# Performance work log

Measured on AMD Instinct MI355X. Metric: run time of the kernel, lower is better.

Reference implementation:

```python
import jax, jax.numpy as jnp
import numpy as np

N = 40000
E = 640000
IN = 128
H = 8
F = 16  # out_features per head; H*F == IN for the residual
NEG_SLOPE = 0.2
BN_EPS = 1e-5
SOFTMAX_EPS = 1e-16


def setup_inputs() -> dict:
    key = jax.random.key(0)
    ks = jax.random.split(key, 7)
    x = jax.random.normal(ks[0], (N, IN), dtype=jnp.float32)
    edge_index = jax.random.randint(ks[1], (2, E), 0, N, dtype=jnp.int32)
    # GATConv parameters (glorot-ish scale)
    W = jax.random.normal(ks[2], (IN, H * F), dtype=jnp.float32) * (1.0 / np.sqrt(IN))
    att_src = jax.random.normal(ks[3], (H, F), dtype=jnp.float32) * (1.0 / np.sqrt(F))
    att_dst = jax.random.normal(ks[4], (H, F), dtype=jnp.float32) * (1.0 / np.sqrt(F))
    bias = jnp.zeros((H * F,), dtype=jnp.float32)
    bn_gamma = jnp.ones((H * F,), dtype=jnp.float32)
    bn_beta = jnp.zeros((H * F,), dtype=jnp.float32)
    return {"x": x, "edge_index": edge_index, "W": W, "att_src": att_src,
            "att_dst": att_dst, "bias": bias, "bn_gamma": bn_gamma, "bn_beta": bn_beta}


def _gat_layer(x, src, dst, W, att_src, att_dst, bias, bn_gamma, bn_beta):
    n = x.shape[0]
    xp = (x @ W).reshape(n, H, F)                      # [N,H,F] transformed features
    a_s = jnp.einsum('nhf,hf->nh', xp, att_src)        # [N,H]
    a_d = jnp.einsum('nhf,hf->nh', xp, att_dst)
    e = jax.nn.leaky_relu(a_s[src] + a_d[dst], NEG_SLOPE)   # [E,H] per-edge logits
    # segment softmax over edges sharing the same destination node
    m = jax.ops.segment_max(e, dst, num_segments=n)    # [N,H]
    m = jnp.where(jnp.isfinite(m), m, 0.0)             # guard isolated nodes
    p = jnp.exp(e - m[dst])
    s = jax.ops.segment_sum(p, dst, num_segments=n)    # [N,H]
    alpha = p / (s[dst] + SOFTMAX_EPS)                 # [E,H]
    # scatter-aggregate messages
    msg = alpha[:, :, None] * xp[src]                  # [E,H,F]
    out = jax.ops.segment_sum(msg, dst, num_segments=n)  # [N,H,F]
    h = out.reshape(n, H * F) + bias
    # BatchNorm1d (training-mode batch statistics, biased variance)
    mean = h.mean(axis=0)
    var = h.var(axis=0)
    h = (h - mean) * jax.lax.rsqrt(var + BN_EPS) * bn_gamma + bn_beta
    h = jax.nn.relu(h)
    return h + x                                        # residual (dropout p=0 -> identity)


def reference(x, edge_index, W, att_src, att_dst, bias, bn_gamma, bn_beta):
    n = x.shape[0]
    loops = jnp.arange(n, dtype=edge_index.dtype)
    src = jnp.concatenate([edge_index[0], loops])       # add self-loops (GATConv default)
    dst = jnp.concatenate([edge_index[1], loops])
    return _gat_layer(x, src, dst, W, att_src, att_dst, bias, bn_gamma, bn_beta)
```

## Files before the change

kernel.cpp:

```cpp
#include <hip/hip_runtime.h>
#include <math.h>


constexpr float NEG_SLOPE = 0.2f;
constexpr float BN_EPS = 1e-5f;
constexpr float SM_EPS = 1e-16f;
constexpr int SLOTS = 96;

typedef __attribute__((ext_vector_type(8))) short short8;
typedef __attribute__((ext_vector_type(4))) float f32x4;

__device__ inline unsigned bf16rne(float f) {
    unsigned b = __float_as_uint(f);
    return (b + 0x7fffu + ((b >> 16) & 1u)) >> 16;
}

__global__ __launch_bounds__(256) void k_init(
    const float* __restrict__ W, const float* __restrict__ att_src,
    const float* __restrict__ att_dst, unsigned short* __restrict__ Wtg,
    int* __restrict__ zbase, int zcount)
{
    int b = blockIdx.x;
    if (b < 64) {
        int idx = b * 256 + threadIdx.x;
        int k = idx >> 7, nc = idx & 127;
        Wtg[nc * 128 + k] = (unsigned short)bf16rne(W[idx]);
    } else if (b < 72) {
        int c = (b - 64) * 16 + (threadIdx.x >> 4);
        int j = threadIdx.x & 15;
        int h = j & 7;
        const float* att = (j < 8) ? att_src : att_dst;
        float v = 0.f;
#pragma unroll
        for (int f = 0; f < 16; ++f)
            v += W[c * 128 + h * 16 + f] * att[h * 16 + f];
        Wtg[(128 + j) * 128 + c] = (unsigned short)bf16rne(v);
    } else {
        int idx = (b - 72) * 256 + threadIdx.x;
        if (idx < zcount) zbase[idx] = 0;
    }
}

__global__ __launch_bounds__(256) void k_gemm(
    const float* __restrict__ x, const unsigned short* __restrict__ Wtg,
    const int* __restrict__ ei, int E,
    unsigned* __restrict__ xpb, float* __restrict__ a_s, float* __restrict__ a_d,
    int* __restrict__ deg, unsigned short* __restrict__ csr_src, int n,
    int ntiles)
{
    if ((int)blockIdx.x >= ntiles) {
        const int t = (blockIdx.x - ntiles) * 256 + threadIdx.x;
        if (t < E) {
            int dst = ei[E + t];
            int src = ei[t];
            int slot = atomicAdd(&deg[dst], 1);
            csr_src[(size_t)dst * SLOTS + slot] = (unsigned short)src;
        } else if (t - E < n) {
            int node = t - E;
            int slot = atomicAdd(&deg[node], 1);
            csr_src[(size_t)node * SLOTS + slot] = (unsigned short)node;
        }
        return;
    }

    const int tid = threadIdx.x;
    const int lane = tid & 63;
    const int wid = tid >> 6;
    const int quad = lane >> 4;
    const int l16 = lane & 15;
    const int row = blockIdx.x * 64 + wid * 16 + l16;

    const float4* x4 = (const float4*)x;
    short8 afrag[4];
#pragma unroll
    for (int kt = 0; kt < 4; ++kt) {
        float4 f0 = make_float4(0.f, 0.f, 0.f, 0.f), f1 = f0;
        if (row < n) {
            f0 = x4[(size_t)row * 32 + kt * 8 + quad * 2];
            f1 = x4[(size_t)row * 32 + kt * 8 + quad * 2 + 1];
        }
        short8 a;
        a[0] = (short)bf16rne(f0.x); a[1] = (short)bf16rne(f0.y);
        a[2] = (short)bf16rne(f0.z); a[3] = (short)bf16rne(f0.w);
        a[4] = (short)bf16rne(f1.x); a[5] = (short)bf16rne(f1.y);
        a[6] = (short)bf16rne(f1.z); a[7] = (short)bf16rne(f1.w);
        afrag[kt] = a;
    }

    f32x4 acc[9];
#pragma unroll
    for (int ct = 0; ct < 9; ++ct) acc[ct] = (f32x4){0.f, 0.f, 0.f, 0.f};

#pragma unroll
    for (int ct = 0; ct < 9; ++ct) {
#pragma unroll
        for (int kt = 0; kt < 4; ++kt) {
            short8 b = *(const short8*)&Wtg[(size_t)(ct * 16 + l16) * 128 + kt * 32 + quad * 8];
            acc[ct] = __builtin_amdgcn_mfma_f32_16x16x32_bf16(afrag[kt], b, acc[ct], 0, 0, 0);
        }
    }

    const int rowbase = blockIdx.x * 64 + wid * 16 + quad * 4;
#pragma unroll
    for (int ct = 0; ct < 8; ++ct) {
#pragma unroll
        for (int r = 0; r < 4; ++r) {
            float val = acc[ct][r];
            float other = __shfl_xor(val, 1);
            int orow = rowbase + r;
            if (!(lane & 1) && orow < n) {
                unsigned u = bf16rne(val) | (bf16rne(other) << 16);
                xpb[(size_t)orow * 64 + ct * 8 + (l16 >> 1)] = u;
            }
        }
    }
#pragma unroll
    for (int r = 0; r < 4; ++r) {
        int orow = rowbase + r;
        if (orow < n) {
            float val = acc[8][r];
            if (l16 < 8) a_s[(size_t)orow * 8 + l16] = val;
            else         a_d[(size_t)orow * 8 + (l16 - 8)] = val;
        }
    }
}

__global__ __launch_bounds__(256) void k_gather(
    const int* __restrict__ deg, const unsigned short* __restrict__ csr_src,
    const float* __restrict__ a_s, const float* __restrict__ a_d,
    const unsigned* __restrict__ xpb, unsigned* __restrict__ aggb, int n)
{
    int node = blockIdx.x * 4 + (threadIdx.x >> 6);
    if (node >= n) return;
    int lane = threadIdx.x & 63;
    int h = lane >> 3;
    float ad = a_d[(size_t)node * 8 + h];
    const unsigned short* rowp = csr_src + (size_t)node * SLOTS;
    int cnt = deg[node];
    float acc0 = 0.f, acc1 = 0.f, s = 0.f;

    for (int slot = 0; slot < cnt; slot += 8) {
        int sx[8]; float w[8]; unsigned u[8];
#pragma unroll
        for (int j = 0; j < 8; ++j) {
            int sj = slot + j;
            sx[j] = rowp[sj < cnt ? sj : cnt - 1];
        }
#pragma unroll
        for (int j = 0; j < 8; ++j) w[j] = a_s[(size_t)sx[j] * 8 + h];
#pragma unroll
        for (int j = 0; j < 8; ++j) u[j] = xpb[(size_t)sx[j] * 64 + lane];
#pragma unroll
        for (int j = 0; j < 8; ++j) {
            float v = w[j] + ad;
            v = v > 0.f ? v : NEG_SLOPE * v;
            float p = __expf(v);
            p = (slot + j < cnt) ? p : 0.f;
            s += p;
            acc0 = fmaf(p, __uint_as_float(u[j] << 16), acc0);
            acc1 = fmaf(p, __uint_as_float(u[j] & 0xffff0000u), acc1);
        }
    }
    float inv = 1.0f / (s + SM_EPS);
    aggb[(size_t)node * 64 + lane] = bf16rne(acc0 * inv) | (bf16rne(acc1 * inv) << 16);
}

__global__ __launch_bounds__(256) void k_bnstats(
    const unsigned* __restrict__ aggb, int n, float* __restrict__ stats)
{
    __shared__ float red[4][256];
    const int cp = threadIdx.x & 63;
    const int rg = threadIdx.x >> 6;
    float s0 = 0.f, s1 = 0.f, q0 = 0.f, q1 = 0.f;
    for (int r = blockIdx.x * 4 + rg; r < n; r += gridDim.x * 4) {
        unsigned u = aggb[(size_t)r * 64 + cp];
        float v0 = __uint_as_float(u << 16);
        float v1 = __uint_as_float(u & 0xffff0000u);
        s0 += v0; q0 += v0 * v0;
        s1 += v1; q1 += v1 * v1;
    }
    red[rg][cp * 2] = s0;       red[rg][cp * 2 + 1] = s1;
    red[rg][128 + cp * 2] = q0; red[rg][128 + cp * 2 + 1] = q1;
    __syncthreads();
    int idx = threadIdx.x;
    float v = red[0][idx] + red[1][idx] + red[2][idx] + red[3][idx];
    if (idx < 128) atomicAdd(&stats[idx], v);
    else           atomicAdd(&stats[128 + (idx - 128)], v);
}

__global__ __launch_bounds__(256) void k_final(
    const unsigned* __restrict__ aggb, const float* __restrict__ gamma,
    const float* __restrict__ beta, const float* __restrict__ stats,
    const float* __restrict__ x, float* __restrict__ out, int n)
{
    int i4 = blockIdx.x * 256 + threadIdx.x;
    int total4 = n * 32;
    if (i4 >= total4) return;
    int c4 = (i4 & 31) * 4;
    float invn = 1.0f / (float)n;
    uint2 au = ((const uint2*)aggb)[i4];
    float av[4] = { __uint_as_float(au.x << 16), __uint_as_float(au.x & 0xffff0000u),
                    __uint_as_float(au.y << 16), __uint_as_float(au.y & 0xffff0000u) };
    float4 xv = ((const float4*)x)[i4];
    float4 o;
#pragma unroll
    for (int j = 0; j < 4; ++j) {
        int c = c4 + j;
        float mean = stats[c] * invn;
        float var = stats[128 + c] * invn - mean * mean;
        float v = (av[j] - mean) * rsqrtf(var + BN_EPS) * gamma[c] + beta[c];
        v = fmaxf(v, 0.f);
        (&o.x)[j] = v + (&xv.x)[j];
    }
    ((float4*)out)[i4] = o;
}

extern "C" void kernel_launch(void* const* d_in, const int* in_sizes, int n_in,
                              void* d_out, int out_size, void* d_ws, size_t ws_size,
                              hipStream_t stream)
{
    const float* x        = (const float*)d_in[0];
    const int*   ei       = (const int*)d_in[1];
    const float* W        = (const float*)d_in[2];
    const float* att_src  = (const float*)d_in[3];
    const float* att_dst  = (const float*)d_in[4];
    const float* bn_gamma = (const float*)d_in[6];
    const float* bn_beta  = (const float*)d_in[7];
    float* out = (float*)d_out;

    const int n = in_sizes[0] / 128;
    const int E = in_sizes[1] / 2;

    float*          stats   = (float*)d_ws;
    int*            deg     = (int*)(stats + 256);
    unsigned short* csr_src = (unsigned short*)(deg + n);
    unsigned short* Wtg     = csr_src + (size_t)n * SLOTS;
    unsigned*       xpb     = (unsigned*)(Wtg + 144 * 128);
    unsigned*       aggb    = xpb + (size_t)n * 64;
    float*          a_s     = (float*)(aggb + (size_t)n * 64);
    float*          a_d     = a_s + (size_t)n * 8;

    const int zcount = 256 + n;
    const int ginit = 72 + (zcount + 255) / 256;
    const int ntiles = (n + 63) >> 6;
    const int eb = (E + n + 255) / 256;
    const int ggemm = ntiles + eb;

    k_init<<<ginit, 256, 0, stream>>>(W, att_src, att_dst, Wtg, (int*)stats, zcount);
    k_gemm<<<ggemm, 256, 0, stream>>>(x, Wtg, ei, E, xpb, a_s, a_d,
                                      deg, csr_src, n, ntiles);
    k_gather<<<(n + 3) / 4, 256, 0, stream>>>(deg, csr_src, a_s, a_d, xpb, aggb, n);
    k_bnstats<<<640, 256, 0, stream>>>(aggb, n, stats);
    k_final<<<(n * 32 + 255) / 256, 256, 0, stream>>>(aggb, bn_gamma, bn_beta,
                                                      stats, x, out, n);
}
```

Baseline: 184.1 us.

## Build CSR via two-level bucket counting sort instead of global atomics into fixed slots

Edge-to-destination grouping is replaced by a bucketed counting sort. A per-block histogram over 64-node buckets is followed by a single-block scan, a scatter into contiguous bucket ranges using shared-memory cursors, and a per-bucket local sort that yields compact per-node row starts and degrees. This removes the per-edge global atomics and the sparse 96-slot padded layout, so the gather reads a dense CSR. The cost is two extra kernel launches, including a serial single-block scan. Packing dst and src into 16 bits each and capping a bucket at 1536 entries only holds for n ≤ 65536 and bounded bucket sizes.

```diff
diff --git a/kernel.cpp b/kernel.cpp
--- a/kernel.cpp
+++ b/kernel.cpp
@@ -5,7 +5,9 @@
 constexpr float NEG_SLOPE = 0.2f;
 constexpr float BN_EPS = 1e-5f;
 constexpr float SM_EPS = 1e-16f;
-constexpr int SLOTS = 96;
+constexpr int NBUCK = 640;
+constexpr int IPB   = 8192;
+constexpr int BCAP  = 1536;
 
 typedef __attribute__((ext_vector_type(8))) short short8;
 typedef __attribute__((ext_vector_type(4))) float f32x4;
@@ -18,7 +20,8 @@
 __global__ __launch_bounds__(256) void k_init(
     const float* __restrict__ W, const float* __restrict__ att_src,
     const float* __restrict__ att_dst, unsigned short* __restrict__ Wtg,
-    int* __restrict__ zbase, int zcount)
+    float* __restrict__ stats, const int* __restrict__ ei, int E, int n,
+    int* __restrict__ ghist, int nba)
 {
     int b = blockIdx.x;
     if (b < 64) {
@@ -35,30 +38,74 @@
         for (int f = 0; f < 16; ++f)
             v += W[c * 128 + h * 16 + f] * att[h * 16 + f];
         Wtg[(128 + j) * 128 + c] = (unsigned short)bf16rne(v);
+    } else if (b == 72) {
+        stats[threadIdx.x] = 0.f;
     } else {
-        int idx = (b - 72) * 256 + threadIdx.x;
-        if (idx < zcount) zbase[idx] = 0;
-    }
+        const int blkA = b - 73;
+        const int T = E + n;
+        __shared__ int lh[NBUCK];
+        for (int i = threadIdx.x; i < NBUCK; i += 256) lh[i] = 0;
+        __syncthreads();
+        const int base = blkA * IPB;
+#pragma unroll
+        for (int i = 0; i < IPB / 256; ++i) {
+            int t = base + i * 256 + threadIdx.x;
+            if (t < T) {
+                int dst = (t < E) ? ei[E + t] : (t - E);
+                atomicAdd(&lh[dst >> 6], 1);
+            }
+        }
+        __syncthreads();
+        for (int i = threadIdx.x; i < NBUCK; i += 256)
+            ghist[i * nba + blkA] = lh[i];
+    }
+}
+
+__global__ __launch_bounds__(1024) void k_scan(int* __restrict__ g, int L)
+{
+    const int td = threadIdx.x;
+    const int ch = (L + 1023) >> 10;
+    const int c0 = td * ch, c1 = min(c0 + ch, L);
+    int s = 0;
+    for (int i = c0; i < c1; ++i) s += g[i];
+    __shared__ int ls[1024];
+    ls[td] = s;
+    __syncthreads();
+    for (int off = 1; off < 1024; off <<= 1) {
+        int v = (td >= off) ? ls[td - off] : 0;
+        __syncthreads();
+        ls[td] += v;
+        __syncthreads();
+    }
+    int run = (td == 0) ? 0 : ls[td - 1];
+    for (int i = c0; i < c1; ++i) { int v = g[i]; g[i] = run; run += v; }
 }
 
 __global__ __launch_bounds__(256) void k_gemm(
     const float* __restrict__ x, const unsigned short* __restrict__ Wtg,
     const int* __restrict__ ei, int E,
     unsigned* __restrict__ xpb, float* __restrict__ a_s, float* __restrict__ a_d,
-    int* __restrict__ deg, unsigned short* __restrict__ csr_src, int n,
-    int ntiles)
-{
+    const int* __restrict__ ghist, unsigned* __restrict__ buck, int n,
+    int ntiles, int nba)
+{
+    __shared__ int cur[NBUCK];
     if ((int)blockIdx.x >= ntiles) {
-        const int t = (blockIdx.x - ntiles) * 256 + threadIdx.x;
-        if (t < E) {
-            int dst = ei[E + t];
-            int src = ei[t];
-            int slot = atomicAdd(&deg[dst], 1);
-            csr_src[(size_t)dst * SLOTS + slot] = (unsigned short)src;
-        } else if (t - E < n) {
-            int node = t - E;
-            int slot = atomicAdd(&deg[node], 1);
-            csr_src[(size_t)node * SLOTS + slot] = (unsigned short)node;
+        const int blkC = blockIdx.x - ntiles;
+        const int T = E + n;
+        for (int i = threadIdx.x; i < NBUCK; i += 256)
+            cur[i] = ghist[i * nba + blkC];
+        __syncthreads();
+        const int base = blkC * IPB;
+#pragma unroll
+        for (int i = 0; i < IPB / 256; ++i) {
+            int t = base + i * 256 + threadIdx.x;
+            if (t < T) {
+                int dst, src;
+                if (t < E) { dst = ei[E + t]; src = ei[t]; }
+                else       { dst = src = t - E; }
+                int pos = atomicAdd(&cur[dst >> 6], 1);
+                buck[pos] = ((unsigned)dst << 16) | (unsigned)src;
+            }
         }
         return;
     }
@@ -95,8 +142,8 @@
     for (int ct = 0; ct < 9; ++ct) {
 #pragma unroll
         for (int kt = 0; kt < 4; ++kt) {
-            short8 b = *(const short8*)&Wtg[(size_t)(ct * 16 + l16) * 128 + kt * 32 + quad * 8];
-            acc[ct] = __builtin_amdgcn_mfma_f32_16x16x32_bf16(afrag[kt], b, acc[ct], 0, 0, 0);
+            short8 bfr = *(const short8*)&Wtg[(size_t)(ct * 16 + l16) * 128 + kt * 32 + quad * 8];
+            acc[ct] = __builtin_amdgcn_mfma_f32_16x16x32_bf16(afrag[kt], bfr, acc[ct], 0, 0, 0);
         }
     }
 
@@ -125,8 +172,49 @@
     }
 }
 
+__global__ __launch_bounds__(256) void k_bfin(
+    const int* __restrict__ ghist, unsigned* __restrict__ buck,
+    int* __restrict__ deg, int* __restrict__ rowst, int n, int T, int nba)
+{
+    const int k = blockIdx.x;
+    const int start = ghist[k * nba];
+    const int end = (k == NBUCK - 1) ? T : ghist[(k + 1) * nba];
+    const int cnt = min(end - start, BCAP);
+    __shared__ unsigned it[BCAP];
+    __shared__ unsigned so[BCAP];
+    __shared__ int h[64], pf[64], curs[64];
+    for (int i = threadIdx.x; i < cnt; i += 256) it[i] = buck[start + i];
+    if (threadIdx.x < 64) h[threadIdx.x] = 0;
+    __syncthreads();
+    for (int i = threadIdx.x; i < cnt; i += 256)
+        atomicAdd(&h[(it[i] >> 16) & 63], 1);
+    __syncthreads();
+    if (threadIdx.x < 64) {
+        int p = 0;
+        for (int j = 0; j < threadIdx.x; ++j) p += h[j];
+        pf[threadIdx.x] = p;
+        curs[threadIdx.x] = p;
+    }
+    __syncthreads();
+    for (int i = threadIdx.x; i < cnt; i += 256) {
+        unsigned v = it[i];
+        int r = atomicAdd(&curs[(v >> 16) & 63], 1);
+        so[r] = v;
+    }
+    __syncthreads();
+    for (int i = threadIdx.x; i < cnt; i += 256) buck[start + i] = so[i];
+    if (threadIdx.x < 64) {
+        int dst = (k << 6) + threadIdx.x;
+        if (dst < n) {
+            deg[dst] = h[threadIdx.x];
+            rowst[dst] = start + pf[threadIdx.x];
+        }
+    }
+}
+
 __global__ __launch_bounds__(256) void k_gather(
-    const int* __restrict__ deg, const unsigned short* __restrict__ csr_src,
+    const int* __restrict__ deg, const int* __restrict__ rowst,
+    const unsigned* __restrict__ buck,
     const float* __restrict__ a_s, const float* __restrict__ a_d,
     const unsigned* __restrict__ xpb, unsigned* __restrict__ aggb, int n)
 {
@@ -135,7 +223,7 @@
     int lane = threadIdx.x & 63;
     int h = lane >> 3;
     float ad = a_d[(size_t)node * 8 + h];
-    const unsigned short* rowp = csr_src + (size_t)node * SLOTS;
+    const unsigned* rowp = buck + rowst[node];
     int cnt = deg[node];
     float acc0 = 0.f, acc1 = 0.f, s = 0.f;
 
@@ -144,7 +232,7 @@
 #pragma unroll
         for (int j = 0; j < 8; ++j) {
             int sj = slot + j;
-            sx[j] = rowp[sj < cnt ? sj : cnt - 1];
+            sx[j] = (int)(rowp[sj < cnt ? sj : cnt - 1] & 0xffffu);
         }
 #pragma unroll
         for (int j = 0; j < 8; ++j) w[j] = a_s[(size_t)sx[j] * 8 + h];
@@ -230,26 +318,33 @@
 
     const int n = in_sizes[0] / 128;
     const int E = in_sizes[1] / 2;
-
-    float*          stats   = (float*)d_ws;
-    int*            deg     = (int*)(stats + 256);
-    unsigned short* csr_src = (unsigned short*)(deg + n);
-    unsigned short* Wtg     = csr_src + (size_t)n * SLOTS;
-    unsigned*       xpb     = (unsigned*)(Wtg + 144 * 128);
-    unsigned*       aggb    = xpb + (size_t)n * 64;
-    float*          a_s     = (float*)(aggb + (size_t)n * 64);
-    float*          a_d     = a_s + (size_t)n * 8;
-
-    const int zcount = 256 + n;
-    const int ginit = 72 + (zcount + 255) / 256;
+    const int T = E + n;
+    const int nba = (T + IPB - 1) / IPB;
+    const int L = NBUCK * nba;
+
+    float*          stats = (float*)d_ws;
+    int*            deg   = (int*)(stats + 256);
+    int*            rowst = deg + n;
+    unsigned short* Wtg   = (unsigned short*)(rowst + n);
+    unsigned*       xpb   = (unsigned*)(Wtg + 144 * 128);
+    unsigned*       aggb  = xpb + (size_t)n * 64;
+    float*          a_s   = (float*)(aggb + (size_t)n * 64);
+    float*          a_d   = a_s + (size_t)n * 8;
+    int*            ghist = (int*)(a_d + (size_t)n * 8);
+    unsigned*       buck  = (unsigned*)(ghist + L);
+
     const int ntiles = (n + 63) >> 6;
-    const int eb = (E + n + 255) / 256;
-    const int ggemm = ntiles + eb;
-
-    k_init<<<ginit, 256, 0, stream>>>(W, att_src, att_dst, Wtg, (int*)stats, zcount);
+    const int ginit = 73 + nba;
+    const int ggemm = ntiles + nba;
+
+    k_init<<<ginit, 256, 0, stream>>>(W, att_src, att_dst, Wtg,
+                                      stats, ei, E, n, ghist, nba);
+    k_scan<<<1, 1024, 0, stream>>>(ghist, L);
     k_gemm<<<ggemm, 256, 0, stream>>>(x, Wtg, ei, E, xpb, a_s, a_d,
-                                      deg, csr_src, n, ntiles);
-    k_gather<<<(n + 3) / 4, 256, 0, stream>>>(deg, csr_src, a_s, a_d, xpb, aggb, n);
+                                      ghist, buck, n, ntiles, nba);
+    k_bfin<<<NBUCK, 256, 0, stream>>>(ghist, buck, deg, rowst, n, T, nba);
+    k_gather<<<(n + 3) / 4, 256, 0, stream>>>(deg, rowst, buck, a_s, a_d,
+                                              xpb, aggb, n);
     k_bnstats<<<640, 256, 0, stream>>>(aggb, n, stats);
     k_final<<<(n * 32 + 255) / 256, 256, 0, stream>>>(aggb, bn_gamma, bn_beta,
                                                       stats, x, out, n);
```

Measured after the change: 267.2 us. 1.45x slower.
